# Performance work log

Hardware: AMD Instinct MI355X
Metric: run time of the kernel (lower is better)

## Reference

```python
import jax, jax.numpy as jnp
import numpy as np

CAT_CARDS = [10, 20, 15, 8, 30, 12, 5, 25, 6, 40, 18, 9]   # categorical_card entries with card > 1 (first 20 entries)
NUM = 32          # num_numerical
NBIN = 8          # categorical_card[:-2] entries with card == 1
NLIKE = 2         # last two categorical_card entries, both card 1
NMASK = NUM + len(CAT_CARDS) + NBIN + NLIKE   # 32 + 22 = 54 mask heads
LAT, HID, B = 128, 1024, 16384
TAU = 1.0
EPS = 1e-20


def setup_inputs() -> dict:
    key = jax.random.key(0)
    ks = jax.random.split(key, 7)
    w = lambda k, sh: (jax.random.normal(k, sh, jnp.float32) * 0.02)
    return {
        "z": jax.random.normal(ks[0], (B, LAT), jnp.float32),
        "W1": w(ks[1], (LAT, HID)), "b1": jnp.zeros((HID,), jnp.float32),
        "W_num": w(ks[2], (HID, NUM)), "b_num": jnp.zeros((NUM,), jnp.float32),
        "W_cat": w(ks[3], (HID, sum(CAT_CARDS))), "b_cat": jnp.zeros((sum(CAT_CARDS),), jnp.float32),
        "W_bin": w(ks[4], (HID, NBIN)), "b_bin": jnp.zeros((NBIN,), jnp.float32),
        "W_like": w(ks[5], (HID, NLIKE)), "b_like": jnp.zeros((NLIKE,), jnp.float32),
        "W_mask": w(ks[6], (HID, NMASK)), "b_mask": jnp.zeros((NMASK,), jnp.float32),
    }


def _gumbel_sigmoid(logits, key, tau=TAU):
    # matches torch: noise~U(0,1); g = -log(-log(noise+eps)+eps); sigmoid((logits+g)/tau); hard=False
    u = jax.random.uniform(key, logits.shape, logits.dtype)
    g = -jnp.log(-jnp.log(u + EPS) + EPS)
    return jax.nn.sigmoid((logits + g) / tau)


def reference(z, W1, b1, W_num, b_num, W_cat, b_cat, W_bin, b_bin, W_like, b_like, W_mask, b_mask):
    nk = jax.random.split(jax.random.key(1), 3)
    h = jax.nn.relu(z @ W1 + b1)                       # [B, HID]
    num_out = h @ W_num + b_num                        # [B, NUM]

    cat_logits = h @ W_cat + b_cat                     # [B, sum(cards)] fused GEMM, then split per head
    splits = np.cumsum(CAT_CARDS)[:-1].tolist()
    cat_out = tuple(jnp.split(cat_logits, splits, axis=1))

    # use_gumbel=True, hard=False: binary / likewise / mask heads get gumbel-sigmoid
    bin_out = _gumbel_sigmoid(h @ W_bin + b_bin, nk[0])      # [B, NBIN]
    like_out = _gumbel_sigmoid(h @ W_like + b_like, nk[1])   # [B, NLIKE]
    mask_out = _gumbel_sigmoid(h @ W_mask + b_mask, nk[2])   # [B, NMASK]

    bins = tuple(bin_out[:, i:i + 1] for i in range(NBIN))
    likes = tuple(like_out[:, i:i + 1] for i in range(NLIKE))
    masks = tuple(mask_out[:, i:i + 1] for i in range(NMASK))
    return (num_out,) + cat_out + bins + likes + masks
```

## Files before the change

kernel.cpp:

```cpp
#include <hip/hip_runtime.h>
#include <stdint.h>

#define B_ROWS 16384
#define LATD   128
#define HIDD   1024

typedef __bf16 bf16x8 __attribute__((ext_vector_type(8)));
typedef float  f32x4  __attribute__((ext_vector_type(4)));
typedef unsigned short ushort8v __attribute__((ext_vector_type(8)));

struct TF2 { unsigned int a, b; };

#define TF_R(x0,x1,r) { x0 += x1; x1 = ((x1 << (r)) | (x1 >> (32 - (r)))); x1 ^= x0; }

__host__ __device__ constexpr TF2 threefry2x32(unsigned k0, unsigned k1, unsigned c0, unsigned c1) {
  unsigned ks2 = k0 ^ k1 ^ 0x1BD11BDAu;
  unsigned x0 = c0 + k0, x1 = c1 + k1;
  TF_R(x0,x1,13) TF_R(x0,x1,15) TF_R(x0,x1,26) TF_R(x0,x1,6)
  x0 += k1;  x1 += ks2 + 1u;
  TF_R(x0,x1,17) TF_R(x0,x1,29) TF_R(x0,x1,16) TF_R(x0,x1,24)
  x0 += ks2; x1 += k0 + 2u;
  TF_R(x0,x1,13) TF_R(x0,x1,15) TF_R(x0,x1,26) TF_R(x0,x1,6)
  x0 += k0;  x1 += k1 + 3u;
  TF_R(x0,x1,17) TF_R(x0,x1,29) TF_R(x0,x1,16) TF_R(x0,x1,24)
  x0 += k1;  x1 += ks2 + 4u;
  TF_R(x0,x1,13) TF_R(x0,x1,15) TF_R(x0,x1,26) TF_R(x0,x1,6)
  x0 += ks2; x1 += k0 + 5u;
  return {x0, x1};
}

constexpr TF2 NK0 = threefry2x32(0u, 1u, 0u, 0u);
constexpr TF2 NK1 = threefry2x32(0u, 1u, 0u, 1u);
constexpr TF2 NK2 = threefry2x32(0u, 1u, 0u, 2u);

__device__ __forceinline__ unsigned short f2bf(float f) {
  unsigned u = __float_as_uint(f);
  return (unsigned short)((u + 0x7fffu + ((u >> 16) & 1u)) >> 16);
}

__global__ void prep_kernel(const float* __restrict__ W1,
                            const float* __restrict__ Wnum, const float* __restrict__ Wcat,
                            const float* __restrict__ Wbin, const float* __restrict__ Wlike,
                            const float* __restrict__ Wmask,
                            const float* __restrict__ bnum, const float* __restrict__ bcat,
                            const float* __restrict__ bbin, const float* __restrict__ blike,
                            const float* __restrict__ bmask,
                            unsigned short* __restrict__ W1p,
                            unsigned short* __restrict__ Wallp,
                            float* __restrict__ ball) {
  int t = blockIdx.x * 256 + threadIdx.x;
  if (t < 16384) {
    int f = t >> 6, l = t & 63;
    int n = (f >> 2) * 16 + (l & 15);
    int kk0 = (f & 3) * 32 + (l >> 4) * 8;
    ushort8v p;
    #pragma unroll
    for (int j = 0; j < 8; ++j) p[j] = f2bf(W1[(size_t)(kk0 + j) * HIDD + n]);
    *(ushort8v*)(W1p + (size_t)t * 8) = p;
  } else if (t < 16384 + 40960) {
    int t2 = t - 16384;
    int g = t2 >> 6, l = t2 & 63;
    int nt = g >> 5, kt = g & 31;
    int n = nt * 16 + (l & 15);
    int kk0 = kt * 32 + (l >> 4) * 8;
    ushort8v p;
    #pragma unroll
    for (int j = 0; j < 8; ++j) {
      int kk = kk0 + j;
      float v = 0.f;
      if (n < 32)       v = Wnum [(size_t)kk * 32  + n];
      else if (n < 230) v = Wcat [(size_t)kk * 198 + (n - 32)];
      else if (n < 238) v = Wbin [(size_t)kk * 8   + (n - 230)];
      else if (n < 240) v = Wlike[(size_t)kk * 2   + (n - 238)];
      else if (n < 294) v = Wmask[(size_t)kk * 54  + (n - 240)];
      p[j] = f2bf(v);
    }
    *(ushort8v*)(Wallp + (size_t)t2 * 8) = p;
  } else if (t < 16384 + 40960 + 320) {
    int n = t - (16384 + 40960);
    float v = 0.f;
    if (n < 32)       v = bnum [n];
    else if (n < 230) v = bcat [n - 32];
    else if (n < 238) v = bbin [n - 230];
    else if (n < 240) v = blike[n - 238];
    else if (n < 294) v = bmask[n - 240];
    ball[n] = v;
  }
}

__global__ __launch_bounds__(512, 2) void decoder_kernel(
    const float* __restrict__ z, const float* __restrict__ b1,
    const unsigned short* __restrict__ W1p, const unsigned short* __restrict__ Wallp,
    const float* __restrict__ ball, float* __restrict__ out) {
  __shared__ __align__(16) unsigned char smem[82176];
  unsigned short* zs  = (unsigned short*)smem;
  unsigned short* hs0 = (unsigned short*)(smem + 17408);
  unsigned short* hs1 = (unsigned short*)(smem + 34816);
  float* outs = (float*)smem;

  const int tid  = threadIdx.x;
  const int lane = tid & 63;
  const int wv   = tid >> 6;
  const int wc   = wv & 3;
  const int wk   = wv >> 2;
  const int l15  = lane & 15;
  const int l4   = lane >> 4;
  const int r0   = blockIdx.x * 64;

  #pragma unroll
  for (int it = 0; it < 2; ++it) {
    int ch  = tid + it * 512;
    int row = ch >> 4;
    int k0  = (ch & 15) * 8;
    const float* src = z + (size_t)(r0 + row) * LATD + k0;
    float4 f0 = *(const float4*)src;
    float4 f1 = *(const float4*)(src + 4);
    ushort8v p;
    p[0] = f2bf(f0.x); p[1] = f2bf(f0.y); p[2] = f2bf(f0.z); p[3] = f2bf(f0.w);
    p[4] = f2bf(f1.x); p[5] = f2bf(f1.y); p[6] = f2bf(f1.z); p[7] = f2bf(f1.w);
    *(ushort8v*)(zs + row * 136 + k0) = p;
  }

  float bb[4][2];
  #pragma unroll
  for (int i = 0; i < 4; ++i)
    #pragma unroll
    for (int ct = 0; ct < 2; ++ct)
      bb[i][ct] = b1[(wk * 4 + i) * 128 + wc * 32 + ct * 16 + l15];
  float bias2[5];
  #pragma unroll
  for (int ct = 0; ct < 5; ++ct) bias2[ct] = ball[wc * 80 + ct * 16 + l15];

  unsigned short* hw = wk ? hs1 : hs0;
  f32x4 acc2[4][5] = {};

  __syncthreads();

  #pragma unroll
  for (int i = 0; i < 4; ++i) {
    const int c = wk * 4 + i;
    bf16x8 wb1[2][4];
    #pragma unroll
    for (int ct = 0; ct < 2; ++ct)
      #pragma unroll
      for (int ks = 0; ks < 4; ++ks)
        wb1[ct][ks] = *(const bf16x8*)(W1p + (size_t)(((c * 8 + wc * 2 + ct) * 4 + ks) * 64 + lane) * 8);
    f32x4 acc1[4][2] = {};
    #pragma unroll
    for (int ks = 0; ks < 4; ++ks) {
      bf16x8 za[4];
      #pragma unroll
      for (int rt = 0; rt < 4; ++rt)
        za[rt] = *(const bf16x8*)(zs + (rt * 16 + l15) * 136 + ks * 32 + l4 * 8);
      #pragma unroll
      for (int rt = 0; rt < 4; ++rt)
        #pragma unroll
        for (int ct = 0; ct < 2; ++ct)
          acc1[rt][ct] = __builtin_amdgcn_mfma_f32_16x16x32_bf16(za[rt], wb1[ct][ks], acc1[rt][ct], 0, 0, 0);
    }
    bf16x8 wb2[5][4];
    #pragma unroll
    for (int ct = 0; ct < 5; ++ct)
      #pragma unroll
      for (int ks = 0; ks < 4; ++ks)
        wb2[ct][ks] = *(const bf16x8*)(Wallp + (size_t)(((wc * 5 + ct) * 32 + c * 4 + ks) * 64 + lane) * 8);
    __syncthreads();
    #pragma unroll
    for (int rt = 0; rt < 4; ++rt)
      #pragma unroll
      for (int ct = 0; ct < 2; ++ct)
        #pragma unroll
        for (int j = 0; j < 4; ++j) {
          float v = fmaxf(acc1[rt][ct][j] + bb[i][ct], 0.f);
          hw[(rt * 16 + l4 * 4 + j) * 136 + wc * 32 + ct * 16 + l15] = f2bf(v);
        }
    __syncthreads();
    #pragma unroll
    for (int ks = 0; ks < 4; ++ks) {
      bf16x8 ha[4];
      #pragma unroll
      for (int rt = 0; rt < 4; ++rt)
        ha[rt] = *(const bf16x8*)(hw + (rt * 16 + l15) * 136 + ks * 32 + l4 * 8);
      #pragma unroll
      for (int rt = 0; rt < 4; ++rt)
        #pragma unroll
        for (int ct = 0; ct < 5; ++ct)
          acc2[rt][ct] = __builtin_amdgcn_mfma_f32_16x16x32_bf16(ha[rt], wb2[ct][ks], acc2[rt][ct], 0, 0, 0);
    }
  }
  __syncthreads();

  if (wk == 0) {
    #pragma unroll
    for (int rt = 0; rt < 4; ++rt)
      #pragma unroll
      for (int ct = 0; ct < 5; ++ct)
        #pragma unroll
        for (int j = 0; j < 4; ++j)
          outs[(rt * 16 + l4 * 4 + j) * 321 + wc * 80 + ct * 16 + l15] = acc2[rt][ct][j] + bias2[ct];
  }
  __syncthreads();
  if (wk == 1) {
    #pragma unroll
    for (int rt = 0; rt < 4; ++rt)
      #pragma unroll
      for (int ct = 0; ct < 5; ++ct)
        #pragma unroll
        for (int j = 0; j < 4; ++j)
          outs[(rt * 16 + l4 * 4 + j) * 321 + wc * 80 + ct * 16 + l15] += acc2[rt][ct][j];
  }
  __syncthreads();

  {
    constexpr int cards[13] = {32,10,20,15,8,30,12,5,25,6,40,18,9};
    constexpr int cbase[13] = {0,32,42,62,77,85,115,127,132,157,163,203,221};
    #pragma unroll
    for (int blk = 0; blk < 13; ++blk) {
      const int card = cards[blk];
      const int cb   = cbase[blk];
      float* gout = out + (size_t)B_ROWS * cb + (size_t)r0 * card;
      for (int v = tid; v < card * 16; v += 512) {
        int g = v * 4;
        float vbuf[4];
        #pragma unroll
        for (int e = 0; e < 4; ++e) {
          int ge = g + e;
          int brow = ge / card;
          int j = ge - brow * card;
          vbuf[e] = outs[brow * 321 + cb + j];
        }
        *(float4*)(gout + g) = *(float4*)vbuf;
      }
    }
  }

  {
    int c = 230 + (tid >> 3);
    unsigned ka, kb; int Nh, head;
    if (c < 238)      { ka = NK0.a; kb = NK0.b; Nh = 8;  head = c - 230; }
    else if (c < 240) { ka = NK1.a; kb = NK1.b; Nh = 2;  head = c - 238; }
    else              { ka = NK2.a; kb = NK2.b; Nh = 54; head = c - 240; }
    #pragma unroll
    for (int q = 0; q < 2; ++q) {
      int rb = (tid & 7) * 4 + q * 32;
      float vbuf[4];
      #pragma unroll
      for (int e = 0; e < 4; ++e) {
        int rl = rb + e;
        float x = outs[rl * 321 + c];
        unsigned j = (unsigned)((r0 + rl) * Nh + head);
        TF2 t = threefry2x32(ka, kb, 0u, j);
        unsigned bits = t.a ^ t.b;
        float u  = __uint_as_float((bits >> 9) | 0x3f800000u) - 1.0f;
        float gn = -logf(-logf(u + 1e-20f) + 1e-20f);
        vbuf[e] = 1.0f / (1.0f + expf(-(x + gn)));
      }
      *(float4*)(out + (size_t)B_ROWS * c + r0 + rb) = *(float4*)vbuf;
    }
  }
}

extern "C" void kernel_launch(void* const* d_in, const int* in_sizes, int n_in,
                              void* d_out, int out_size, void* d_ws, size_t ws_size,
                              hipStream_t stream) {
  const float* z     = (const float*)d_in[0];
  const float* W1    = (const float*)d_in[1];
  const float* b1    = (const float*)d_in[2];
  const float* Wnum  = (const float*)d_in[3];
  const float* bnum  = (const float*)d_in[4];
  const float* Wcat  = (const float*)d_in[5];
  const float* bcat  = (const float*)d_in[6];
  const float* Wbin  = (const float*)d_in[7];
  const float* bbin  = (const float*)d_in[8];
  const float* Wlike = (const float*)d_in[9];
  const float* blike = (const float*)d_in[10];
  const float* Wmask = (const float*)d_in[11];
  const float* bmask = (const float*)d_in[12];

  unsigned short* W1p   = (unsigned short*)d_ws;
  unsigned short* Wallp = W1p + 131072;
  float*          ball  = (float*)(Wallp + 327680);

  const int total = 16384 + 40960 + 320;
  prep_kernel<<<(total + 255) / 256, 256, 0, stream>>>(
      W1, Wnum, Wcat, Wbin, Wlike, Wmask, bnum, bcat, bbin, blike, bmask,
      W1p, Wallp, ball);

  decoder_kernel<<<B_ROWS / 64, 512, 0, stream>>>(
      z, b1, W1p, Wallp, ball, (float*)d_out);
}
```

Before: 34.12 us.

## Double-buffer hidden tiles, prefetch W1 fragments, pad LDS stride, use nontemporal I/O

Each wave group now writes its hidden tile into one of two alternating LDS buffers. This removes one of the two workgroup barriers per chunk. The next chunk's W1 fragments are prefetched while the current one is consumed, and the second-layer weights are loaded earlier. The LDS row stride changes from 136 to 140 to reduce bank conflicts, and the z loads and output stores become nontemporal. In exchange the kernel uses more LDS (89.6KB), which may affect two-blocks-per-CU occupancy, and it holds more registers.

```diff
diff --git a/kernel.cpp b/kernel.cpp
--- a/kernel.cpp
+++ b/kernel.cpp
@@ -4,10 +4,18 @@
 #define B_ROWS 16384
 #define LATD   128
 #define HIDD   1024
+#define ZSTR   140
 
 typedef __bf16 bf16x8 __attribute__((ext_vector_type(8)));
 typedef float  f32x4  __attribute__((ext_vector_type(4)));
+typedef float  f32x4v __attribute__((ext_vector_type(4)));
 typedef unsigned short ushort8v __attribute__((ext_vector_type(8)));
+
+#define WG_BARRIER() do {                                          \
+    asm volatile("s_waitcnt lgkmcnt(0)" ::: "memory");             \
+    __builtin_amdgcn_s_barrier();                                  \
+    asm volatile("" ::: "memory");                                 \
+  } while (0)
 
 struct TF2 { unsigned int a, b; };
 
@@ -92,10 +100,8 @@
     const float* __restrict__ z, const float* __restrict__ b1,
     const unsigned short* __restrict__ W1p, const unsigned short* __restrict__ Wallp,
     const float* __restrict__ ball, float* __restrict__ out) {
-  __shared__ __align__(16) unsigned char smem[82176];
-  unsigned short* zs  = (unsigned short*)smem;
-  unsigned short* hs0 = (unsigned short*)(smem + 17408);
-  unsigned short* hs1 = (unsigned short*)(smem + 34816);
+  __shared__ __align__(16) unsigned char smem[89600];
+  unsigned short* zs = (unsigned short*)smem;
   float* outs = (float*)smem;
 
   const int tid  = threadIdx.x;
@@ -107,18 +113,21 @@
   const int l4   = lane >> 4;
   const int r0   = blockIdx.x * 64;
 
+  unsigned short* H0 = (unsigned short*)(smem + 17920 + wk * 35840);
+  unsigned short* H1 = H0 + 8960;
+
   #pragma unroll
   for (int it = 0; it < 2; ++it) {
     int ch  = tid + it * 512;
     int row = ch >> 4;
     int k0  = (ch & 15) * 8;
     const float* src = z + (size_t)(r0 + row) * LATD + k0;
-    float4 f0 = *(const float4*)src;
-    float4 f1 = *(const float4*)(src + 4);
+    f32x4v f0 = __builtin_nontemporal_load((const f32x4v*)src);
+    f32x4v f1 = __builtin_nontemporal_load((const f32x4v*)(src + 4));
     ushort8v p;
-    p[0] = f2bf(f0.x); p[1] = f2bf(f0.y); p[2] = f2bf(f0.z); p[3] = f2bf(f0.w);
-    p[4] = f2bf(f1.x); p[5] = f2bf(f1.y); p[6] = f2bf(f1.z); p[7] = f2bf(f1.w);
-    *(ushort8v*)(zs + row * 136 + k0) = p;
+    p[0] = f2bf(f0[0]); p[1] = f2bf(f0[1]); p[2] = f2bf(f0[2]); p[3] = f2bf(f0[3]);
+    p[4] = f2bf(f1[0]); p[5] = f2bf(f1[1]); p[6] = f2bf(f1[2]); p[7] = f2bf(f1[3]);
+    *(ushort8v*)(zs + row * ZSTR + k0) = p;
   }
 
   float bb[4][2];
@@ -127,68 +136,86 @@
     #pragma unroll
     for (int ct = 0; ct < 2; ++ct)
       bb[i][ct] = b1[(wk * 4 + i) * 128 + wc * 32 + ct * 16 + l15];
+
+  bf16x8 wb1[2][4];
+  {
+    const int c0 = wk * 4;
+    #pragma unroll
+    for (int ct = 0; ct < 2; ++ct)
+      #pragma unroll
+      for (int ks = 0; ks < 4; ++ks)
+        wb1[ct][ks] = *(const bf16x8*)(W1p + (size_t)(((c0 * 8 + wc * 2 + ct) * 4 + ks) * 64 + lane) * 8);
+  }
+
+  f32x4 acc2[4][5] = {};
+
+  WG_BARRIER();
+
+  #pragma unroll
+  for (int i = 0; i < 4; ++i) {
+    const int c = wk * 4 + i;
+    bf16x8 wb2[5][4];
+    #pragma unroll
+    for (int ct = 0; ct < 5; ++ct)
+      #pragma unroll
+      for (int ks = 0; ks < 4; ++ks)
+        wb2[ct][ks] = *(const bf16x8*)(Wallp + (size_t)(((wc * 5 + ct) * 32 + c * 4 + ks) * 64 + lane) * 8);
+
+    f32x4 acc1[4][2] = {};
+    #pragma unroll
+    for (int ks = 0; ks < 4; ++ks) {
+      bf16x8 za[4];
+      #pragma unroll
+      for (int rt = 0; rt < 4; ++rt)
+        za[rt] = *(const bf16x8*)(zs + (rt * 16 + l15) * ZSTR + ks * 32 + l4 * 8);
+      #pragma unroll
+      for (int rt = 0; rt < 4; ++rt)
+        #pragma unroll
+        for (int ct = 0; ct < 2; ++ct)
+          acc1[rt][ct] = __builtin_amdgcn_mfma_f32_16x16x32_bf16(za[rt], wb1[ct][ks], acc1[rt][ct], 0, 0, 0);
+    }
+
+    unsigned short* hw = (i & 1) ? H1 : H0;
+    #pragma unroll
+    for (int rt = 0; rt < 4; ++rt)
+      #pragma unroll
+      for (int ct = 0; ct < 2; ++ct)
+        #pragma unroll
+        for (int j = 0; j < 4; ++j) {
+          float v = fmaxf(acc1[rt][ct][j] + bb[i][ct], 0.f);
+          hw[(rt * 16 + l4 * 4 + j) * ZSTR + wc * 32 + ct * 16 + l15] = f2bf(v);
+        }
+
+    if (i < 3) {
+      const int cn = c + 1;
+      #pragma unroll
+      for (int ct = 0; ct < 2; ++ct)
+        #pragma unroll
+        for (int ks = 0; ks < 4; ++ks)
+          wb1[ct][ks] = *(const bf16x8*)(W1p + (size_t)(((cn * 8 + wc * 2 + ct) * 4 + ks) * 64 + lane) * 8);
+    }
+
+    WG_BARRIER();
+
+    #pragma unroll
+    for (int ks = 0; ks < 4; ++ks) {
+      bf16x8 ha[4];
+      #pragma unroll
+      for (int rt = 0; rt < 4; ++rt)
+        ha[rt] = *(const bf16x8*)(hw + (rt * 16 + l15) * ZSTR + ks * 32 + l4 * 8);
+      #pragma unroll
+      for (int rt = 0; rt < 4; ++rt)
+        #pragma unroll
+        for (int ct = 0; ct < 5; ++ct)
+          acc2[rt][ct] = __builtin_amdgcn_mfma_f32_16x16x32_bf16(ha[rt], wb2[ct][ks], acc2[rt][ct], 0, 0, 0);
+    }
+  }
+
+  __syncthreads();
+
   float bias2[5];
   #pragma unroll
   for (int ct = 0; ct < 5; ++ct) bias2[ct] = ball[wc * 80 + ct * 16 + l15];
-
-  unsigned short* hw = wk ? hs1 : hs0;
-  f32x4 acc2[4][5] = {};
-
-  __syncthreads();
-
-  #pragma unroll
-  for (int i = 0; i < 4; ++i) {
-    const int c = wk * 4 + i;
-    bf16x8 wb1[2][4];
-    #pragma unroll
-    for (int ct = 0; ct < 2; ++ct)
-      #pragma unroll
-      for (int ks = 0; ks < 4; ++ks)
-        wb1[ct][ks] = *(const bf16x8*)(W1p + (size_t)(((c * 8 + wc * 2 + ct) * 4 + ks) * 64 + lane) * 8);
-    f32x4 acc1[4][2] = {};
-    #pragma unroll
-    for (int ks = 0; ks < 4; ++ks) {
-      bf16x8 za[4];
-      #pragma unroll
-      for (int rt = 0; rt < 4; ++rt)
-        za[rt] = *(const bf16x8*)(zs + (rt * 16 + l15) * 136 + ks * 32 + l4 * 8);
-      #pragma unroll
-      for (int rt = 0; rt < 4; ++rt)
-        #pragma unroll
-        for (int ct = 0; ct < 2; ++ct)
-          acc1[rt][ct] = __builtin_amdgcn_mfma_f32_16x16x32_bf16(za[rt], wb1[ct][ks], acc1[rt][ct], 0, 0, 0);
-    }
-    bf16x8 wb2[5][4];
-    #pragma unroll
-    for (int ct = 0; ct < 5; ++ct)
-      #pragma unroll
-      for (int ks = 0; ks < 4; ++ks)
-        wb2[ct][ks] = *(const bf16x8*)(Wallp + (size_t)(((wc * 5 + ct) * 32 + c * 4 + ks) * 64 + lane) * 8);
-    __syncthreads();
-    #pragma unroll
-    for (int rt = 0; rt < 4; ++rt)
-      #pragma unroll
-      for (int ct = 0; ct < 2; ++ct)
-        #pragma unroll
-        for (int j = 0; j < 4; ++j) {
-          float v = fmaxf(acc1[rt][ct][j] + bb[i][ct], 0.f);
-          hw[(rt * 16 + l4 * 4 + j) * 136 + wc * 32 + ct * 16 + l15] = f2bf(v);
-        }
-    __syncthreads();
-    #pragma unroll
-    for (int ks = 0; ks < 4; ++ks) {
-      bf16x8 ha[4];
-      #pragma unroll
-      for (int rt = 0; rt < 4; ++rt)
-        ha[rt] = *(const bf16x8*)(hw + (rt * 16 + l15) * 136 + ks * 32 + l4 * 8);
-      #pragma unroll
-      for (int rt = 0; rt < 4; ++rt)
-        #pragma unroll
-        for (int ct = 0; ct < 5; ++ct)
-          acc2[rt][ct] = __builtin_amdgcn_mfma_f32_16x16x32_bf16(ha[rt], wb2[ct][ks], acc2[rt][ct], 0, 0, 0);
-    }
-  }
-  __syncthreads();
 
   if (wk == 0) {
     #pragma unroll
@@ -221,7 +248,7 @@
       float* gout = out + (size_t)B_ROWS * cb + (size_t)r0 * card;
       for (int v = tid; v < card * 16; v += 512) {
         int g = v * 4;
-        float vbuf[4];
+        f32x4v vbuf;
         #pragma unroll
         for (int e = 0; e < 4; ++e) {
           int ge = g + e;
@@ -229,7 +256,7 @@
           int j = ge - brow * card;
           vbuf[e] = outs[brow * 321 + cb + j];
         }
-        *(float4*)(gout + g) = *(float4*)vbuf;
+        __builtin_nontemporal_store(vbuf, (f32x4v*)(gout + g));
       }
     }
   }
@@ -243,7 +270,7 @@
     #pragma unroll
     for (int q = 0; q < 2; ++q) {
       int rb = (tid & 7) * 4 + q * 32;
-      float vbuf[4];
+      f32x4v vbuf;
       #pragma unroll
       for (int e = 0; e < 4; ++e) {
         int rl = rb + e;
@@ -255,7 +282,7 @@
         float gn = -logf(-logf(u + 1e-20f) + 1e-20f);
         vbuf[e] = 1.0f / (1.0f + expf(-(x + gn)));
       }
-      *(float4*)(out + (size_t)B_ROWS * c + r0 + rb) = *(float4*)vbuf;
+      __builtin_nontemporal_store(vbuf, (f32x4v*)(out + (size_t)B_ROWS * c + r0 + rb));
     }
   }
 }
```

Measured after the change: 50.55 us. +48.2%, slower.

## Split fused decoder into hidden-layer and output-head kernels via workspace

Applied to the files above, without the earlier changes.

Replaces the single fused decoder with two kernels. The first computes relu(z@W1+b1) in bf16 and writes it to a 32 MB workspace in an MFMA-ready tiled layout. The second streams those tiles into LDS with double-buffered global_load_lds, runs the head GEMM with 10 waves each owning 32 columns, then does the same scatter and gumbel epilogue. This trades the fused kernel's on-chip h reuse for a global round trip of the hidden activations, in exchange for a simpler, better-pipelined second GEMM and more parallelism in the first. The old path stays as a fallback when the workspace is too small.

```diff
diff --git a/kernel.cpp b/kernel.cpp
--- a/kernel.cpp
+++ b/kernel.cpp
@@ -7,7 +7,9 @@
 
 typedef __bf16 bf16x8 __attribute__((ext_vector_type(8)));
 typedef float  f32x4  __attribute__((ext_vector_type(4)));
+typedef float  f32x4v __attribute__((ext_vector_type(4)));
 typedef unsigned short ushort8v __attribute__((ext_vector_type(8)));
+typedef unsigned int   uint2v   __attribute__((ext_vector_type(2)));
 
 struct TF2 { unsigned int a, b; };
 
@@ -88,6 +90,191 @@
   }
 }
 
+__global__ __launch_bounds__(256, 4) void h_kernel(
+    const float* __restrict__ z, const float* __restrict__ b1,
+    const unsigned short* __restrict__ W1p, unsigned char* __restrict__ hws) {
+  const int tid = threadIdx.x;
+  const int lane = tid & 63;
+  const int w    = tid >> 6;
+  const int l15  = lane & 15;
+  const int l4   = lane >> 4;
+  const int g    = blockIdx.x;
+  const int rb   = (g >> 1) * 32;
+  const int hcb  = (g & 1) * 512 + w * 128;
+
+  bf16x8 zb[2][4];
+  #pragma unroll
+  for (int rt = 0; rt < 2; ++rt)
+    #pragma unroll
+    for (int ks = 0; ks < 4; ++ks) {
+      const float* src = z + (size_t)(rb + rt * 16 + l15) * LATD + ks * 32 + l4 * 8;
+      f32x4 f0 = *(const f32x4*)src;
+      f32x4 f1 = *(const f32x4*)(src + 4);
+      bf16x8 p;
+      p[0] = (__bf16)f0[0]; p[1] = (__bf16)f0[1]; p[2] = (__bf16)f0[2]; p[3] = (__bf16)f0[3];
+      p[4] = (__bf16)f1[0]; p[5] = (__bf16)f1[1]; p[6] = (__bf16)f1[2]; p[7] = (__bf16)f1[3];
+      zb[rt][ks] = p;
+    }
+
+  f32x4 acc[8][2] = {};
+  #pragma unroll
+  for (int t = 0; t < 8; ++t) {
+    #pragma unroll
+    for (int ks = 0; ks < 4; ++ks) {
+      bf16x8 wA = *(const bf16x8*)(W1p + ((size_t)((hcb >> 4) + t) * 4 + ks) * 512 + lane * 8);
+      #pragma unroll
+      for (int rt = 0; rt < 2; ++rt)
+        acc[t][rt] = __builtin_amdgcn_mfma_f32_16x16x32_bf16(wA, zb[rt][ks], acc[t][rt], 0, 0, 0);
+    }
+  }
+
+  const size_t tile_base = ((size_t)(rb >> 6) * 8 + (hcb >> 7)) * 16384;
+  const int rhalf_base = (rb & 32) >> 4;
+  #pragma unroll
+  for (int t = 0; t < 8; ++t) {
+    f32x4 bias = *(const f32x4*)(b1 + hcb + t * 16 + l4 * 4);
+    #pragma unroll
+    for (int rt = 0; rt < 2; ++rt) {
+      float v0 = fmaxf(acc[t][rt][0] + bias[0], 0.f);
+      float v1 = fmaxf(acc[t][rt][1] + bias[1], 0.f);
+      float v2 = fmaxf(acc[t][rt][2] + bias[2], 0.f);
+      float v3 = fmaxf(acc[t][rt][3] + bias[3], 0.f);
+      uint2v u;
+      u[0] = (unsigned)f2bf(v0) | ((unsigned)f2bf(v1) << 16);
+      u[1] = (unsigned)f2bf(v2) | ((unsigned)f2bf(v3) << 16);
+      int rhalf = rhalf_base + rt;
+      int byte = (((t >> 1) * 4 + rhalf) * 1024)
+               + l15 * 16
+               + (((t & 1) * 2 + (l4 >> 1)) * 256)
+               + ((l4 & 1) * 8);
+      *(uint2v*)(hws + tile_base + byte) = u;
+    }
+  }
+}
+
+__global__ __launch_bounds__(640, 2) void out_kernel(
+    const unsigned char* __restrict__ hws, const unsigned short* __restrict__ Wallp,
+    const float* __restrict__ ball, float* __restrict__ out) {
+  __shared__ __align__(16) unsigned char smem[114944];
+  float* outs = (float*)(smem + 32768);
+
+  const int tid  = threadIdx.x;
+  const int lane = tid & 63;
+  const int wv   = tid >> 6;
+  const int l15  = lane & 15;
+  const int l4   = lane >> 4;
+  const int rb   = blockIdx.x * 64;
+  const int cb   = wv * 32;
+  const size_t hblk = (size_t)blockIdx.x * 8 * 16384;
+
+  const int s0 = (wv < 6) ? wv * 2 : 12 + (wv - 6);
+  const int ns = (wv < 6) ? 2 : 1;
+
+  f32x4 acc[4][2] = {};
+
+  for (int i = 0; i < ns; ++i) {
+    int s = s0 + i;
+    const unsigned char* src = hws + hblk + (size_t)s * 1024 + lane * 16;
+    __builtin_amdgcn_global_load_lds(
+        (const __attribute__((address_space(1))) unsigned int*)src,
+        (__attribute__((address_space(3))) unsigned int*)(smem + s * 1024), 16, 0, 0);
+  }
+
+  for (int c = 0; c < 8; ++c) {
+    __syncthreads();
+    if (c < 7) {
+      unsigned char* dbuf = smem + ((c + 1) & 1) * 16384;
+      for (int i = 0; i < ns; ++i) {
+        int s = s0 + i;
+        const unsigned char* src = hws + hblk + (size_t)(c + 1) * 16384 + s * 1024 + lane * 16;
+        __builtin_amdgcn_global_load_lds(
+            (const __attribute__((address_space(1))) unsigned int*)src,
+            (__attribute__((address_space(3))) unsigned int*)(dbuf + s * 1024), 16, 0, 0);
+      }
+    }
+    bf16x8 wb[2][4];
+    #pragma unroll
+    for (int ct = 0; ct < 2; ++ct)
+      #pragma unroll
+      for (int ks = 0; ks < 4; ++ks)
+        wb[ct][ks] = *(const bf16x8*)(Wallp +
+            ((size_t)(((cb >> 4) + ct) * 32 + c * 4 + ks) * 64 + lane) * 8);
+    const unsigned char* buf = smem + (c & 1) * 16384;
+    #pragma unroll
+    for (int ks = 0; ks < 4; ++ks) {
+      bf16x8 ha[4];
+      #pragma unroll
+      for (int rt = 0; rt < 4; ++rt)
+        ha[rt] = *(const bf16x8*)(buf + (ks * 4 + rt) * 1024 + lane * 16);
+      #pragma unroll
+      for (int rt = 0; rt < 4; ++rt)
+        #pragma unroll
+        for (int ct = 0; ct < 2; ++ct)
+          acc[rt][ct] = __builtin_amdgcn_mfma_f32_16x16x32_bf16(ha[rt], wb[ct][ks], acc[rt][ct], 0, 0, 0);
+    }
+  }
+
+  float bias2[2];
+  #pragma unroll
+  for (int ct = 0; ct < 2; ++ct) bias2[ct] = ball[cb + ct * 16 + l15];
+  #pragma unroll
+  for (int rt = 0; rt < 4; ++rt)
+    #pragma unroll
+    for (int ct = 0; ct < 2; ++ct)
+      #pragma unroll
+      for (int j = 0; j < 4; ++j)
+        outs[(rt * 16 + l4 * 4 + j) * 321 + cb + ct * 16 + l15] = acc[rt][ct][j] + bias2[ct];
+  __syncthreads();
+
+  {
+    constexpr int cards[13] = {32,10,20,15,8,30,12,5,25,6,40,18,9};
+    constexpr int cbase[13] = {0,32,42,62,77,85,115,127,132,157,163,203,221};
+    #pragma unroll
+    for (int blk = 0; blk < 13; ++blk) {
+      const int card = cards[blk];
+      const int cbs  = cbase[blk];
+      float* gout = out + (size_t)B_ROWS * cbs + (size_t)rb * card;
+      for (int v = tid; v < card * 16; v += 640) {
+        int gg = v * 4;
+        f32x4v vbuf;
+        #pragma unroll
+        for (int e = 0; e < 4; ++e) {
+          int ge = gg + e;
+          int brow = ge / card;
+          int j = ge - brow * card;
+          vbuf[e] = outs[brow * 321 + cbs + j];
+        }
+        *(f32x4v*)(gout + gg) = vbuf;
+      }
+    }
+  }
+
+  if (tid < 512) {
+    int c = 230 + (tid >> 3);
+    unsigned ka, kb; int Nh, head;
+    if (c < 238)      { ka = NK0.a; kb = NK0.b; Nh = 8;  head = c - 230; }
+    else if (c < 240) { ka = NK1.a; kb = NK1.b; Nh = 2;  head = c - 238; }
+    else              { ka = NK2.a; kb = NK2.b; Nh = 54; head = c - 240; }
+    #pragma unroll
+    for (int q = 0; q < 2; ++q) {
+      int rq = (tid & 7) * 4 + q * 32;
+      f32x4v vbuf;
+      #pragma unroll
+      for (int e = 0; e < 4; ++e) {
+        int rl = rq + e;
+        float x = outs[rl * 321 + c];
+        unsigned j = (unsigned)((rb + rl) * Nh + head);
+        TF2 t = threefry2x32(ka, kb, 0u, j);
+        unsigned bits = t.a ^ t.b;
+        float u  = __uint_as_float((bits >> 9) | 0x3f800000u) - 1.0f;
+        float gn = -logf(-logf(u + 1e-20f) + 1e-20f);
+        vbuf[e] = 1.0f / (1.0f + expf(-(x + gn)));
+      }
+      *(f32x4v*)(out + (size_t)B_ROWS * c + rb + rq) = vbuf;
+    }
+  }
+}
+
 __global__ __launch_bounds__(512, 2) void decoder_kernel(
     const float* __restrict__ z, const float* __restrict__ b1,
     const unsigned short* __restrict__ W1p, const unsigned short* __restrict__ Wallp,
@@ -113,11 +300,11 @@
     int row = ch >> 4;
     int k0  = (ch & 15) * 8;
     const float* src = z + (size_t)(r0 + row) * LATD + k0;
-    float4 f0 = *(const float4*)src;
-    float4 f1 = *(const float4*)(src + 4);
+    f32x4 f0 = *(const f32x4*)src;
+    f32x4 f1 = *(const f32x4*)(src + 4);
     ushort8v p;
-    p[0] = f2bf(f0.x); p[1] = f2bf(f0.y); p[2] = f2bf(f0.z); p[3] = f2bf(f0.w);
-    p[4] = f2bf(f1.x); p[5] = f2bf(f1.y); p[6] = f2bf(f1.z); p[7] = f2bf(f1.w);
+    p[0] = f2bf(f0[0]); p[1] = f2bf(f0[1]); p[2] = f2bf(f0[2]); p[3] = f2bf(f0[3]);
+    p[4] = f2bf(f1[0]); p[5] = f2bf(f1[1]); p[6] = f2bf(f1[2]); p[7] = f2bf(f1[3]);
     *(ushort8v*)(zs + row * 136 + k0) = p;
   }
 
@@ -133,7 +320,6 @@
 
   unsigned short* hw = wk ? hs1 : hs0;
   f32x4 acc2[4][5] = {};
-
   __syncthreads();
 
   #pragma unroll
@@ -217,23 +403,22 @@
     #pragma unroll
     for (int blk = 0; blk < 13; ++blk) {
       const int card = cards[blk];
-      const int cb   = cbase[blk];
-      float* gout = out + (size_t)B_ROWS * cb + (size_t)r0 * card;
+      const int cbs  = cbase[blk];
+      float* gout = out + (size_t)B_ROWS * cbs + (size_t)r0 * card;
       for (int v = tid; v < card * 16; v += 512) {
-        int g = v * 4;
-        float vbuf[4];
+        int gg = v * 4;
+        f32x4v vbuf;
         #pragma unroll
         for (int e = 0; e < 4; ++e) {
-          int ge = g + e;
+          int ge = gg + e;
           int brow = ge / card;
           int j = ge - brow * card;
-          vbuf[e] = outs[brow * 321 + cb + j];
+          vbuf[e] = outs[brow * 321 + cbs + j];
         }
-        *(float4*)(gout + g) = *(float4*)vbuf;
+        *(f32x4v*)(gout + gg) = vbuf;
       }
     }
   }
-
   {
     int c = 230 + (tid >> 3);
     unsigned ka, kb; int Nh, head;
@@ -242,11 +427,11 @@
     else              { ka = NK2.a; kb = NK2.b; Nh = 54; head = c - 240; }
     #pragma unroll
     for (int q = 0; q < 2; ++q) {
-      int rb = (tid & 7) * 4 + q * 32;
-      float vbuf[4];
+      int rq = (tid & 7) * 4 + q * 32;
+      f32x4v vbuf;
       #pragma unroll
       for (int e = 0; e < 4; ++e) {
-        int rl = rb + e;
+        int rl = rq + e;
         float x = outs[rl * 321 + c];
         unsigned j = (unsigned)((r0 + rl) * Nh + head);
         TF2 t = threefry2x32(ka, kb, 0u, j);
@@ -255,7 +440,7 @@
         float gn = -logf(-logf(u + 1e-20f) + 1e-20f);
         vbuf[e] = 1.0f / (1.0f + expf(-(x + gn)));
       }
-      *(float4*)(out + (size_t)B_ROWS * c + r0 + rb) = *(float4*)vbuf;
+      *(f32x4v*)(out + (size_t)B_ROWS * c + r0 + rq) = vbuf;
     }
   }
 }
@@ -280,12 +465,19 @@
   unsigned short* W1p   = (unsigned short*)d_ws;
   unsigned short* Wallp = W1p + 131072;
   float*          ball  = (float*)(Wallp + 327680);
+  const size_t HOFF = 1u << 20;
+  unsigned char*  hws   = (unsigned char*)d_ws + HOFF;
 
   const int total = 16384 + 40960 + 320;
   prep_kernel<<<(total + 255) / 256, 256, 0, stream>>>(
       W1, Wnum, Wcat, Wbin, Wlike, Wmask, bnum, bcat, bbin, blike, bmask,
       W1p, Wallp, ball);
 
-  decoder_kernel<<<B_ROWS / 64, 512, 0, stream>>>(
-      z, b1, W1p, Wallp, ball, (float*)d_out);
-}
+  if (ws_size >= HOFF + (size_t)32 * 1024 * 1024) {
+    h_kernel<<<1024, 256, 0, stream>>>(z, b1, W1p, hws);
+    out_kernel<<<256, 640, 0, stream>>>(hws, Wallp, ball, (float*)d_out);
+  } else {
+    decoder_kernel<<<B_ROWS / 64, 512, 0, stream>>>(
+        z, b1, W1p, Wallp, ball, (float*)d_out);
+  }
+}
```

Result: slower. 53.37 us (+56.4%).
